# Performance work log

Measured on AMD Instinct MI355X. Metric: run time of the kernel, lower is better.

Reference implementation:

```python
import jax, jax.numpy as jnp
import numpy as np

SEQ, DM, STATE, BATCH = 1024, 512, 16, 8
D2 = 2 * DM
EPS = 1e-5


def rmsnorm(x, w):
    return x * jax.lax.rsqrt(jnp.mean(x * x, axis=-1, keepdims=True) + EPS) * w


def setup_inputs() -> dict:
    key = jax.random.key(0)
    ks = jax.random.split(key, 16)
    def lin(k, i, o):
        k1, k2 = jax.random.split(k)
        s = 1.0 / np.sqrt(i)
        return (jax.random.uniform(k1, (i, o), minval=-s, maxval=s),
                jax.random.uniform(k2, (o,), minval=-s, maxval=s))
    inp_w, inp_b = lin(ks[0], DM, D2)
    convlin_w, convlin_b = lin(ks[1], D2, D2)
    fc1_w, fc1_b = lin(ks[2], D2, D2)
    fc2_w, fc2_b = lin(ks[3], D2, STATE)
    fc3_w, fc3_b = lin(ks[4], D2, STATE)
    D_w, D_b = lin(ks[5], DM, D2)
    out_w, _ = lin(ks[6], D2, DM)
    out_b = jnp.ones((DM,))  # nn.init.constant_(out_proj.bias, 1.0)
    # Conv1d(seq_len, seq_len, k=3): weight (out_ch=SEQ, in_ch=SEQ, 3)
    s = 1.0 / np.sqrt(SEQ * 3)
    conv_w = jax.random.uniform(ks[7], (SEQ, SEQ, 3), minval=-s, maxval=s)
    conv_b = jax.random.uniform(ks[8], (SEQ,), minval=-s, maxval=s)
    norm_w = jnp.ones((DM,))
    x = jax.random.normal(ks[9], (BATCH, SEQ, DM))
    return dict(x=x, norm_w=norm_w, inp_w=inp_w, inp_b=inp_b, conv_w=conv_w,
                conv_b=conv_b, convlin_w=convlin_w, convlin_b=convlin_b,
                fc1_w=fc1_w, fc1_b=fc1_b, fc2_w=fc2_w, fc2_b=fc2_b,
                fc3_w=fc3_w, fc3_b=fc3_b, D_w=D_w, D_b=D_b,
                out_w=out_w, out_b=out_b)


def reference(x, norm_w, inp_w, inp_b, conv_w, conv_b, convlin_w, convlin_b,
              fc1_w, fc1_b, fc2_w, fc2_b, fc3_w, fc3_b, D_w, D_b, out_w, out_b):
    xn = rmsnorm(x, norm_w)                                  # (b, L, d)
    x_proj = xn @ inp_w + inp_b                              # (b, L, 2d)
    # Conv1d over channels=seq_len, spatial=2d, padding=1
    x_conv = jax.lax.conv_general_dilated(
        x_proj, conv_w, window_strides=(1,), padding=[(1, 1)],
        dimension_numbers=('NCH', 'OIH', 'NCH')) + conv_b[None, :, None]
    x_conv_out = jax.nn.silu(x_conv) @ convlin_w + convlin_b  # (b, L, 2d)
    # S6: h starts at zero so dA term vanishes; y = x*delta*sum_n(B*C)
    u = x_conv_out
    B = u @ fc2_w + fc2_b                                     # (b, L, n)
    C = u @ fc3_w + fc3_b                                     # (b, L, n)
    delta = jax.nn.softplus(u @ fc1_w + fc1_b)                # (b, L, 2d)
    bc = jnp.sum(B * C, axis=-1, keepdims=True)               # (b, L, 1)
    x_ssm = u * delta * bc                                    # (b, L, 2d)
    x_act = jax.nn.silu(x_ssm)
    x_residual = jax.nn.silu(xn @ D_w + D_b)
    return (x_residual * x_act) @ out_w + out_b               # (b, L, d)
```

## Files before the change

### kernel.cpp

```cpp
#include <hip/hip_runtime.h>
#include <hip/hip_bf16.h>

#define SEQ 1024
#define DM 512
#define D2 1024
#define NSTATE 16
#define BATCH 8
#define ROWS (BATCH * SEQ)
#define EPSF 1e-5f

typedef __attribute__((ext_vector_type(8))) short bf16x8;
typedef __attribute__((ext_vector_type(4))) float f32x4;

#define AS1 __attribute__((address_space(1)))
#define AS3 __attribute__((address_space(3)))

__device__ __forceinline__ void gll16(const void* g, void* l) {
    __builtin_amdgcn_global_load_lds(
        (const AS1 unsigned int*)(uintptr_t)g,
        (AS3 unsigned int*)(unsigned int)(uintptr_t)l, 16, 0, 0);
}

__device__ __forceinline__ float sigmoidf_(float x) {
    return 1.f / (1.f + __expf(-x));
}

__global__ __launch_bounds__(256) void tcvt_k(const float* __restrict__ src,
                                              __hip_bfloat16* __restrict__ dst,
                                              int R, int C) {
    __shared__ float tile[32][33];
    int c0 = blockIdx.x * 32, r0 = blockIdx.y * 32;
    int tx = threadIdx.x & 31, ty = threadIdx.x >> 5;
#pragma unroll
    for (int p = 0; p < 4; ++p) {
        int r = r0 + ty + p * 8, c = c0 + tx;
        if (r < R && c < C) tile[ty + p * 8][tx] = src[(size_t)r * C + c];
    }
    __syncthreads();
#pragma unroll
    for (int p = 0; p < 4; ++p) {
        int c = c0 + ty + p * 8, r = r0 + tx;
        if (r < R && c < C)
            dst[(size_t)c * R + r] = __float2bfloat16(tile[tx][ty + p * 8]);
    }
}

__global__ __launch_bounds__(256) void convw_k(const float* __restrict__ cw,
                                               __hip_bfloat16* __restrict__ wk) {
    int idx = blockIdx.x * 256 + threadIdx.x;
    float a = cw[(size_t)idx * 3 + 0];
    float b = cw[(size_t)idx * 3 + 1];
    float c = cw[(size_t)idx * 3 + 2];
    wk[idx] = __float2bfloat16(a);
    wk[(size_t)SEQ * SEQ + idx] = __float2bfloat16(b);
    wk[(size_t)2 * SEQ * SEQ + idx] = __float2bfloat16(c);
}

__global__ __launch_bounds__(256) void rmsnorm_k(
    const float* __restrict__ x, const float* __restrict__ w,
    __hip_bfloat16* __restrict__ o) {
    int row = blockIdx.x;
    const float* xr = x + (size_t)row * DM;
    __hip_bfloat16* orow = o + (size_t)row * DM;
    int t = threadIdx.x;
    float v0 = xr[t];
    float v1 = xr[t + 256];
    float ss = v0 * v0 + v1 * v1;
#pragma unroll
    for (int off = 32; off; off >>= 1) ss += __shfl_down(ss, off, 64);
    __shared__ float parts[4];
    if ((t & 63) == 0) parts[t >> 6] = ss;
    __syncthreads();
    float tot = parts[0] + parts[1] + parts[2] + parts[3];
    float rs = rsqrtf(tot * (1.f / DM) + EPSF);
    orow[t] = __float2bfloat16(v0 * rs * w[t]);
    orow[t + 256] = __float2bfloat16(v1 * rs * w[t + 256]);
}

template <int EPI>
__global__ __launch_bounds__(256) void mgemm(
    const __hip_bfloat16* __restrict__ A, const __hip_bfloat16* __restrict__ Bt,
    const float* __restrict__ bias, void* __restrict__ outp,
    const __hip_bfloat16* __restrict__ uptr,
    const __hip_bfloat16* __restrict__ resid, const float* __restrict__ bcv,
    int M, int N, int K) {
    __shared__ __align__(16) __hip_bfloat16 As[3][64 * 32];
    __shared__ __align__(16) __hip_bfloat16 Bs[3][128 * 32];
    const int nbx = gridDim.x;
    int lin = blockIdx.y * nbx + blockIdx.x;
    int chunk = (nbx * gridDim.y) >> 3;
    int wg = (lin & 7) * chunk + (lin >> 3);
    const int n0 = (wg % nbx) * 128, m0 = (wg / nbx) * 64;
    const int t = threadIdx.x, lane = t & 63, w = t >> 6;
    const int wr = w >> 1, wc = w & 1;
    const int l15 = lane & 15, l4 = lane >> 4;

    const int rA = t >> 2, cA = (t & 3) ^ ((rA >> 1) & 3);
    const int b1 = 256 + t, rB1 = b1 >> 2, cB1 = (b1 & 3) ^ ((rB1 >> 1) & 3);
    const __hip_bfloat16* gA = A + (size_t)(m0 + rA) * K + cA * 8;
    const __hip_bfloat16* gB0 = Bt + (size_t)(n0 + rA) * K + cA * 8;
    const __hip_bfloat16* gB1 = Bt + (size_t)(n0 + rB1) * K + cB1 * 8;
    const int d0 = (w * 64) * 8, d1 = (256 + w * 64) * 8;

    int offA[2], offB[4];
#pragma unroll
    for (int i = 0; i < 2; ++i) {
        int ra = wr * 32 + i * 16 + l15;
        offA[i] = (ra * 4 + (l4 ^ ((ra >> 1) & 3))) * 8;
    }
#pragma unroll
    for (int j = 0; j < 4; ++j) {
        int rb = wc * 64 + j * 16 + l15;
        offB[j] = (rb * 4 + (l4 ^ ((rb >> 1) & 3))) * 8;
    }

#define MSTAGE(BUF, K0)                  \
    {                                    \
        gll16(gA + (K0), &As[BUF][d0]);  \
        gll16(gB0 + (K0), &Bs[BUF][d0]); \
        gll16(gB1 + (K0), &Bs[BUF][d1]); \
    }

    f32x4 acc[2][4] = {};
    const int NT = K >> 5;
    unsigned curb = 0, nxtb = 1, thdb = 2;
    MSTAGE(0, 0);
    MSTAGE(1, 32);
    asm volatile("s_waitcnt vmcnt(3)" ::: "memory");
    __builtin_amdgcn_s_barrier();
    __builtin_amdgcn_sched_barrier(0);

#pragma unroll 1
    for (int kt = 0; kt < NT; ++kt) {
        const bool st = (kt + 2 < NT);
        if (st) MSTAGE(thdb, (kt + 2) * 32);
        bf16x8 af[2], bv[4];
#pragma unroll
        for (int i = 0; i < 2; ++i) af[i] = *(const bf16x8*)&As[curb][offA[i]];
#pragma unroll
        for (int j = 0; j < 4; ++j) bv[j] = *(const bf16x8*)&Bs[curb][offB[j]];
#pragma unroll
        for (int i = 0; i < 2; ++i)
#pragma unroll
            for (int j = 0; j < 4; ++j)
                acc[i][j] = __builtin_amdgcn_mfma_f32_16x16x32_bf16(
                    af[i], bv[j], acc[i][j], 0, 0, 0);
        if (kt + 1 < NT) {
            if (st)
                asm volatile("s_waitcnt vmcnt(3)" ::: "memory");
            else
                asm volatile("s_waitcnt vmcnt(0)" ::: "memory");
            __builtin_amdgcn_s_barrier();
            __builtin_amdgcn_sched_barrier(0);
        }
        unsigned tb = curb;
        curb = nxtb;
        nxtb = thdb;
        thdb = tb;
    }
#undef MSTAGE

    const int mb = m0 + wr * 32, nb = n0 + wc * 64;
#pragma unroll
    for (int i = 0; i < 2; ++i) {
#pragma unroll
        for (int j = 0; j < 4; ++j) {
            int ngl = nb + j * 16 + l15;
            if (EPI == 6) {
                int bz = ngl >> 10, tl = ngl & 1023;
#pragma unroll
                for (int r = 0; r < 4; ++r) {
                    int mg = mb + i * 16 + l4 * 4 + r;
                    float c = acc[i][j][r] + bias[mg];
                    ((__hip_bfloat16*)outp)[(size_t)bz * D2 * SEQ +
                                            (size_t)mg * SEQ + tl] =
                        __float2bfloat16(c);
                }
            } else {
                float bj = bias[ngl];
#pragma unroll
                for (int r = 0; r < 4; ++r) {
                    int mg = mb + i * 16 + l4 * 4 + r;
                    size_t ro = (size_t)mg * N + ngl;
                    float c = acc[i][j][r] + bj;
                    if (EPI == 1) {
                        ((__hip_bfloat16*)outp)[ro] = __float2bfloat16(c);
                    } else if (EPI == 2) {
                        ((__hip_bfloat16*)outp)[ro] =
                            __float2bfloat16(c * sigmoidf_(c));
                    } else if (EPI == 3) {
                        float sp = (c > 20.f) ? c : log1pf(__expf(c));
                        float xs = __bfloat162float(uptr[ro]) * sp * bcv[mg];
                        float v = __bfloat162float(resid[ro]) *
                                  (xs * sigmoidf_(xs));
                        ((__hip_bfloat16*)outp)[ro] = __float2bfloat16(v);
                    } else {
                        ((float*)outp)[ro] = c;
                    }
                }
            }
        }
    }
}

__global__ __launch_bounds__(256) void conv_mfma(
    const __hip_bfloat16* __restrict__ wk,
    const __hip_bfloat16* __restrict__ Xt,
    const float* __restrict__ cb, __hip_bfloat16* __restrict__ outp) {
    __shared__ __align__(16) __hip_bfloat16 Ws[2][3][64 * 32];
    __shared__ __align__(16) __hip_bfloat16 Xs[2][128 * 32];
    __shared__ __align__(16) __hip_bfloat16 Xh[2][SEQ];
    int lin = blockIdx.x + 8 * blockIdx.y + 128 * blockIdx.z;
    int wg = (lin & 7) * 128 + (lin >> 3);
    const int n0 = (wg & 7) * 128;
    const int m0 = ((wg >> 3) & 15) * 64;
    const int z = wg >> 7;
    const int t = threadIdx.x, lane = t & 63, w = t >> 6;
    const int wr = w >> 1, wc = w & 1;
    const int l15 = lane & 15, l4 = lane >> 4;
    const __hip_bfloat16* Xtb = Xt + (size_t)z * D2 * SEQ;

    {
        int which = t >> 7;
        int col = (t & 127) * 8;
        int h = n0 - 1 + which * 129;
        uint4 v = make_uint4(0u, 0u, 0u, 0u);
        if (h >= 0 && h < D2)
            v = *(const uint4*)(Xtb + (size_t)h * SEQ + col);
        *(uint4*)&Xh[which][col] = v;
    }

    const int rA = t >> 2, cA = (t & 3) ^ ((rA >> 1) & 3);
    const int b1 = 256 + t, rB1 = b1 >> 2, cB1 = (b1 & 3) ^ ((rB1 >> 1) & 3);
    const __hip_bfloat16* wsrc[3];
#pragma unroll
    for (int tp = 0; tp < 3; ++tp)
        wsrc[tp] = wk + (size_t)tp * SEQ * SEQ + (size_t)(m0 + rA) * SEQ +
                   cA * 8;
    const __hip_bfloat16* xsrc0 = Xtb + (size_t)(n0 + rA) * SEQ + cA * 8;
    const __hip_bfloat16* xsrc1 = Xtb + (size_t)(n0 + rB1) * SEQ + cB1 * 8;
    const int d0 = (w * 64) * 8, d1 = (256 + w * 64) * 8;

    int offA[2];
#pragma unroll
    for (int i = 0; i < 2; ++i) {
        int ra = wr * 32 + i * 16 + l15;
        offA[i] = (ra * 4 + (l4 ^ ((ra >> 1) & 3))) * 8;
    }

#define CSTAGE(BUF, K0)                            \
    {                                              \
        gll16(wsrc[0] + (K0), &Ws[BUF][0][d0]);    \
        gll16(wsrc[1] + (K0), &Ws[BUF][1][d0]);    \
        gll16(wsrc[2] + (K0), &Ws[BUF][2][d0]);    \
        gll16(xsrc0 + (K0), &Xs[BUF][d0]);         \
        gll16(xsrc1 + (K0), &Xs[BUF][d1]);         \
    }

    f32x4 acc[2][4] = {};
    CSTAGE(0, 0);
    asm volatile("s_waitcnt vmcnt(0) lgkmcnt(0)" ::: "memory");
    __builtin_amdgcn_s_barrier();
    __builtin_amdgcn_sched_barrier(0);

#pragma unroll 1
    for (int kt = 0; kt < 32; ++kt) {
        const int k0 = kt * 32;
        const int buf = kt & 1;
        if (kt + 1 < 32) CSTAGE(buf ^ 1, (kt + 1) * 32);
        bf16x8 aw[3][2];
#pragma unroll
        for (int tp = 0; tp < 3; ++tp)
#pragma unroll
            for (int i = 0; i < 2; ++i)
                aw[tp][i] = *(const bf16x8*)&Ws[buf][tp][offA[i]];
#pragma unroll
        for (int j = 0; j < 4; ++j) {
#pragma unroll
            for (int tp = 0; tp < 3; ++tp) {
                int rb = wc * 64 + j * 16 + l15 + tp;
                int r = rb - 1;
                const __hip_bfloat16* src =
                    &Xs[buf][(r * 4 + (l4 ^ ((r >> 1) & 3))) * 8];
                if (rb == 0) src = &Xh[0][k0 + l4 * 8];
                if (rb == 129) src = &Xh[1][k0 + l4 * 8];
                bf16x8 bvx = *(const bf16x8*)src;
#pragma unroll
                for (int i = 0; i < 2; ++i)
                    acc[i][j] = __builtin_amdgcn_mfma_f32_16x16x32_bf16(
                        aw[tp][i], bvx, acc[i][j], 0, 0, 0);
            }
        }
        if (kt + 1 < 32) {
            asm volatile("s_waitcnt vmcnt(0)" ::: "memory");
            __builtin_amdgcn_s_barrier();
            __builtin_amdgcn_sched_barrier(0);
        }
    }
#undef CSTAGE

    const int mb = m0 + wr * 32, nb = n0 + wc * 64;
    size_t ob = (size_t)z * SEQ * D2;
#pragma unroll
    for (int i = 0; i < 2; ++i)
#pragma unroll
        for (int j = 0; j < 4; ++j)
#pragma unroll
            for (int r = 0; r < 4; ++r) {
                int mg = mb + i * 16 + l4 * 4 + r;
                int ng = nb + j * 16 + l15;
                float c = acc[i][j][r] + cb[mg];
                outp[ob + (size_t)mg * D2 + ng] =
                    __float2bfloat16(c * sigmoidf_(c));
            }
}

__global__ __launch_bounds__(256) void bc2_k(
    const __hip_bfloat16* __restrict__ u, const __hip_bfloat16* __restrict__ fcT,
    const float* __restrict__ b2, const float* __restrict__ b3,
    float* __restrict__ bc) {
    __shared__ __align__(16) __hip_bfloat16 Bl[32 * 1024];
    __shared__ __align__(16) __hip_bfloat16 As[3][128 * 32];
    const int m0 = blockIdx.x * 128;
    const int t = threadIdx.x, lane = t & 63, w = t >> 6;
    const int l15 = lane & 15, l4 = lane >> 4;

#pragma unroll
    for (int it = 0; it < 16; ++it) {
        int q = it * 256 + t;
        int n = q >> 7, blk = q & 127;
        uint4 v = *(const uint4*)(fcT + (size_t)n * 1024 + blk * 8);
        *(uint4*)&Bl[(n * 128 + (blk ^ (n & 7))) * 8] = v;
    }

    const int r0_ = t >> 2, c0_ = (t & 3) ^ ((r0_ >> 1) & 3);
    const int bq = 256 + t, r1_ = bq >> 2, c1_ = (bq & 3) ^ ((r1_ >> 1) & 3);
    const __hip_bfloat16* gA0 = u + (size_t)(m0 + r0_) * 1024 + c0_ * 8;
    const __hip_bfloat16* gA1 = u + (size_t)(m0 + r1_) * 1024 + c1_ * 8;
    const int d0 = (w * 64) * 8, d1 = (256 + w * 64) * 8;

    int offA[2];
#pragma unroll
    for (int i = 0; i < 2; ++i) {
        int ra = w * 32 + i * 16 + l15;
        offA[i] = (ra * 4 + (l4 ^ ((ra >> 1) & 3))) * 8;
    }

#define BSTAGE(BUF, K0)                  \
    {                                    \
        gll16(gA0 + (K0), &As[BUF][d0]); \
        gll16(gA1 + (K0), &As[BUF][d1]); \
    }

    f32x4 acc[2][2] = {};
    unsigned curb = 0, nxtb = 1, thdb = 2;
    BSTAGE(0, 0);
    BSTAGE(1, 32);
    asm volatile("s_waitcnt vmcnt(2)" ::: "memory");
    __builtin_amdgcn_s_barrier();
    __builtin_amdgcn_sched_barrier(0);

#pragma unroll 1
    for (int kt = 0; kt < 32; ++kt) {
        const bool st = (kt + 2 < 32);
        if (st) BSTAGE(thdb, (kt + 2) * 32);
        bf16x8 af[2], bf[2];
#pragma unroll
        for (int i = 0; i < 2; ++i) af[i] = *(const bf16x8*)&As[curb][offA[i]];
#pragma unroll
        for (int nj = 0; nj < 2; ++nj) {
            int n = nj * 16 + l15;
            int blk = (kt * 4 + l4) ^ (n & 7);
            bf[nj] = *(const bf16x8*)&Bl[(n * 128 + blk) * 8];
        }
#pragma unroll
        for (int i = 0; i < 2; ++i)
#pragma unroll
            for (int nj = 0; nj < 2; ++nj)
                acc[i][nj] = __builtin_amdgcn_mfma_f32_16x16x32_bf16(
                    af[i], bf[nj], acc[i][nj], 0, 0, 0);
        if (kt + 1 < 32) {
            if (st)
                asm volatile("s_waitcnt vmcnt(2)" ::: "memory");
            else
                asm volatile("s_waitcnt vmcnt(0)" ::: "memory");
            __builtin_amdgcn_s_barrier();
            __builtin_amdgcn_sched_barrier(0);
        }
        unsigned tb = curb;
        curb = nxtb;
        nxtb = thdb;
        thdb = tb;
    }
#undef BSTAGE

    float bb2 = b2[l15], bb3 = b3[l15];
#pragma unroll
    for (int i = 0; i < 2; ++i)
#pragma unroll
        for (int r = 0; r < 4; ++r) {
            float Bv = acc[i][0][r] + bb2;
            float Cv = acc[i][1][r] + bb3;
            float p = Bv * Cv;
            p += __shfl_xor(p, 1, 64);
            p += __shfl_xor(p, 2, 64);
            p += __shfl_xor(p, 4, 64);
            p += __shfl_xor(p, 8, 64);
            if (l15 == 0)
                bc[m0 + w * 32 + i * 16 + l4 * 4 + r] = p;
        }
}

extern "C" void kernel_launch(void* const* d_in, const int* in_sizes, int n_in,
                              void* d_out, int out_size, void* d_ws,
                              size_t ws_size, hipStream_t stream) {
    const float* x = (const float*)d_in[0];
    const float* norm_w = (const float*)d_in[1];
    const float* inp_w = (const float*)d_in[2];
    const float* inp_b = (const float*)d_in[3];
    const float* conv_w = (const float*)d_in[4];
    const float* conv_b = (const float*)d_in[5];
    const float* convlin_w = (const float*)d_in[6];
    const float* convlin_b = (const float*)d_in[7];
    const float* fc1_w = (const float*)d_in[8];
    const float* fc1_b = (const float*)d_in[9];
    const float* fc2_w = (const float*)d_in[10];
    const float* fc2_b = (const float*)d_in[11];
    const float* fc3_w = (const float*)d_in[12];
    const float* fc3_b = (const float*)d_in[13];
    const float* D_w = (const float*)d_in[14];
    const float* D_b = (const float*)d_in[15];
    const float* out_w = (const float*)d_in[16];
    const float* out_b = (const float*)d_in[17];
    float* out = (float*)d_out;

    __hip_bfloat16* xnb = (__hip_bfloat16*)d_ws;
    __hip_bfloat16* xt = xnb + (size_t)ROWS * DM;
    __hip_bfloat16* cvo = xt + (size_t)BATCH * D2 * SEQ;
    __hip_bfloat16* u = cvo + (size_t)ROWS * D2;
    __hip_bfloat16* resid = u + (size_t)ROWS * D2;
    __hip_bfloat16* inpT = resid + (size_t)ROWS * D2;
    __hip_bfloat16* DT = inpT + (size_t)D2 * DM;
    __hip_bfloat16* clT = DT + (size_t)D2 * DM;
    __hip_bfloat16* fc1T = clT + (size_t)D2 * D2;
    __hip_bfloat16* outT = fc1T + (size_t)D2 * D2;
    __hip_bfloat16* wk = outT + (size_t)DM * D2;
    __hip_bfloat16* fcT = wk + (size_t)3 * SEQ * SEQ;
    float* bcb = (float*)(fcT + (size_t)32 * D2);

    tcvt_k<<<dim3(D2 / 32, DM / 32), 256, 0, stream>>>(inp_w, inpT, DM, D2);
    tcvt_k<<<dim3(D2 / 32, DM / 32), 256, 0, stream>>>(D_w, DT, DM, D2);
    tcvt_k<<<dim3(D2 / 32, D2 / 32), 256, 0, stream>>>(convlin_w, clT, D2, D2);
    tcvt_k<<<dim3(D2 / 32, D2 / 32), 256, 0, stream>>>(fc1_w, fc1T, D2, D2);
    tcvt_k<<<dim3(DM / 32, D2 / 32), 256, 0, stream>>>(out_w, outT, D2, DM);
    tcvt_k<<<dim3(1, D2 / 32), 256, 0, stream>>>(fc2_w, fcT, D2, NSTATE);
    tcvt_k<<<dim3(1, D2 / 32), 256, 0, stream>>>(fc3_w, fcT + (size_t)16 * D2,
                                                 D2, NSTATE);
    convw_k<<<SEQ * SEQ / 256, 256, 0, stream>>>(conv_w, wk);
    rmsnorm_k<<<ROWS, 256, 0, stream>>>(x, norm_w, xnb);
    mgemm<6><<<dim3(ROWS / 128, D2 / 64), 256, 0, stream>>>(
        inpT, xnb, inp_b, xt, nullptr, nullptr, nullptr, D2, ROWS, DM);
    mgemm<2><<<dim3(D2 / 128, ROWS / 64), 256, 0, stream>>>(
        xnb, DT, D_b, resid, nullptr, nullptr, nullptr, ROWS, D2, DM);
    conv_mfma<<<dim3(D2 / 128, SEQ / 64, BATCH), 256, 0, stream>>>(
        wk, xt, conv_b, cvo);
    mgemm<1><<<dim3(D2 / 128, ROWS / 64), 256, 0, stream>>>(
        cvo, clT, convlin_b, u, nullptr, nullptr, nullptr, ROWS, D2, D2);
    bc2_k<<<ROWS / 128, 256, 0, stream>>>(u, fcT, fc2_b, fc3_b, bcb);
    mgemm<3><<<dim3(D2 / 128, ROWS / 64), 256, 0, stream>>>(
        u, fc1T, fc1_b, cvo, u, resid, bcb, ROWS, D2, D2);
    mgemm<4><<<dim3(DM / 128, ROWS / 64), 256, 0, stream>>>(
        cvo, outT, out_b, out, nullptr, nullptr, nullptr, ROWS, DM, D2);
}
```

Measured before the change: 257.7 us.

## Use BK=64 double-buffered GEMM pipeline instead of BK=32 triple-buffer

The GEMM mainloop K-tile grows from 32 to 64 and the LDS pipeline drops from three buffers to two, with an 8-chunk XOR swizzle in place of the 4-chunk one. Each iteration now issues six 16-byte global-to-LDS loads and sixteen MFMAs, which halves the number of barriers and loop iterations per K. In exchange there is only one tile of prefetch lookahead, and vmcnt(0) waits fully each iteration, so less memory latency can be hidden. LDS use per block also rises.

Measured after the change: 250.7 us. 2.7% less time.

```diff
diff --git a/kernel.cpp b/kernel.cpp
--- a/kernel.cpp
+++ b/kernel.cpp
@@ -84,8 +84,8 @@
     const __hip_bfloat16* __restrict__ uptr,
     const __hip_bfloat16* __restrict__ resid, const float* __restrict__ bcv,
     int M, int N, int K) {
-    __shared__ __align__(16) __hip_bfloat16 As[3][64 * 32];
-    __shared__ __align__(16) __hip_bfloat16 Bs[3][128 * 32];
+    __shared__ __align__(16) __hip_bfloat16 As[2][64 * 64];
+    __shared__ __align__(16) __hip_bfloat16 Bs[2][128 * 64];
     const int nbx = gridDim.x;
     int lin = blockIdx.y * nbx + blockIdx.x;
     int chunk = (nbx * gridDim.y) >> 3;
@@ -95,68 +95,83 @@
     const int wr = w >> 1, wc = w & 1;
     const int l15 = lane & 15, l4 = lane >> 4;
 
-    const int rA = t >> 2, cA = (t & 3) ^ ((rA >> 1) & 3);
-    const int b1 = 256 + t, rB1 = b1 >> 2, cB1 = (b1 & 3) ^ ((rB1 >> 1) & 3);
-    const __hip_bfloat16* gA = A + (size_t)(m0 + rA) * K + cA * 8;
-    const __hip_bfloat16* gB0 = Bt + (size_t)(n0 + rA) * K + cA * 8;
-    const __hip_bfloat16* gB1 = Bt + (size_t)(n0 + rB1) * K + cB1 * 8;
-    const int d0 = (w * 64) * 8, d1 = (256 + w * 64) * 8;
-
-    int offA[2], offB[4];
+    const __hip_bfloat16* srcA[2];
+    const __hip_bfloat16* srcB[4];
+    int dA[2], dB[4];
+#pragma unroll
+    for (int p = 0; p < 2; ++p) {
+        int q = p * 256 + t, r = q >> 3, cs = (q & 7) ^ (r & 7);
+        srcA[p] = A + (size_t)(m0 + r) * K + cs * 8;
+        dA[p] = (p * 256 + w * 64) * 8;
+    }
+#pragma unroll
+    for (int p = 0; p < 4; ++p) {
+        int q = p * 256 + t, r = q >> 3, cs = (q & 7) ^ (r & 7);
+        srcB[p] = Bt + (size_t)(n0 + r) * K + cs * 8;
+        dB[p] = (p * 256 + w * 64) * 8;
+    }
+
+    int offA[2][2], offB[4][2];
 #pragma unroll
     for (int i = 0; i < 2; ++i) {
         int ra = wr * 32 + i * 16 + l15;
-        offA[i] = (ra * 4 + (l4 ^ ((ra >> 1) & 3))) * 8;
+#pragma unroll
+        for (int h = 0; h < 2; ++h)
+            offA[i][h] = (ra * 8 + ((h * 4 + l4) ^ (ra & 7))) * 8;
     }
 #pragma unroll
     for (int j = 0; j < 4; ++j) {
         int rb = wc * 64 + j * 16 + l15;
-        offB[j] = (rb * 4 + (l4 ^ ((rb >> 1) & 3))) * 8;
-    }
-
-#define MSTAGE(BUF, K0)                  \
-    {                                    \
-        gll16(gA + (K0), &As[BUF][d0]);  \
-        gll16(gB0 + (K0), &Bs[BUF][d0]); \
-        gll16(gB1 + (K0), &Bs[BUF][d1]); \
+#pragma unroll
+        for (int h = 0; h < 2; ++h)
+            offB[j][h] = (rb * 8 + ((h * 4 + l4) ^ (rb & 7))) * 8;
+    }
+
+#define MSTAGE(BUF, K0)                      \
+    {                                        \
+        gll16(srcA[0] + (K0), &As[BUF][dA[0]]); \
+        gll16(srcA[1] + (K0), &As[BUF][dA[1]]); \
+        gll16(srcB[0] + (K0), &Bs[BUF][dB[0]]); \
+        gll16(srcB[1] + (K0), &Bs[BUF][dB[1]]); \
+        gll16(srcB[2] + (K0), &Bs[BUF][dB[2]]); \
+        gll16(srcB[3] + (K0), &Bs[BUF][dB[3]]); \
     }
 
     f32x4 acc[2][4] = {};
-    const int NT = K >> 5;
-    unsigned curb = 0, nxtb = 1, thdb = 2;
+    const int NT = K >> 6;
     MSTAGE(0, 0);
-    MSTAGE(1, 32);
-    asm volatile("s_waitcnt vmcnt(3)" ::: "memory");
+    asm volatile("s_waitcnt vmcnt(0)" ::: "memory");
     __builtin_amdgcn_s_barrier();
     __builtin_amdgcn_sched_barrier(0);
 
 #pragma unroll 1
     for (int kt = 0; kt < NT; ++kt) {
-        const bool st = (kt + 2 < NT);
-        if (st) MSTAGE(thdb, (kt + 2) * 32);
-        bf16x8 af[2], bv[4];
-#pragma unroll
-        for (int i = 0; i < 2; ++i) af[i] = *(const bf16x8*)&As[curb][offA[i]];
-#pragma unroll
-        for (int j = 0; j < 4; ++j) bv[j] = *(const bf16x8*)&Bs[curb][offB[j]];
+        const int buf = kt & 1;
+        if (kt + 1 < NT) MSTAGE(buf ^ 1, (kt + 1) * 64);
+        bf16x8 af[2][2], bv[4][2];
 #pragma unroll
         for (int i = 0; i < 2; ++i)
 #pragma unroll
-            for (int j = 0; j < 4; ++j)
-                acc[i][j] = __builtin_amdgcn_mfma_f32_16x16x32_bf16(
-                    af[i], bv[j], acc[i][j], 0, 0, 0);
+            for (int h = 0; h < 2; ++h)
+                af[i][h] = *(const bf16x8*)&As[buf][offA[i][h]];
+#pragma unroll
+        for (int j = 0; j < 4; ++j)
+#pragma unroll
+            for (int h = 0; h < 2; ++h)
+                bv[j][h] = *(const bf16x8*)&Bs[buf][offB[j][h]];
+#pragma unroll
+        for (int h = 0; h < 2; ++h)
+#pragma unroll
+            for (int i = 0; i < 2; ++i)
+#pragma unroll
+                for (int j = 0; j < 4; ++j)
+                    acc[i][j] = __builtin_amdgcn_mfma_f32_16x16x32_bf16(
+                        af[i][h], bv[j][h], acc[i][j], 0, 0, 0);
         if (kt + 1 < NT) {
-            if (st)
-                asm volatile("s_waitcnt vmcnt(3)" ::: "memory");
-            else
-                asm volatile("s_waitcnt vmcnt(0)" ::: "memory");
+            asm volatile("s_waitcnt vmcnt(0)" ::: "memory");
             __builtin_amdgcn_s_barrier();
             __builtin_amdgcn_sched_barrier(0);
         }
-        unsigned tb = curb;
-        curb = nxtb;
-        nxtb = thdb;
-        thdb = tb;
     }
 #undef MSTAGE
 
```
